# Optimization experiments

Measured on AMD Instinct MI355X. Metric: run time of the kernel, lower is better.

Reference implementation:

```python
import jax, jax.numpy as jnp
import numpy as np

N_STATE = 8
N_NEURONS = 64
EPS = 1e-4


def setup_inputs() -> dict:
    key = jax.random.key(0)
    ks = jax.random.split(key, 10)
    B = 524288
    return {
        "hidden_state": jax.random.normal(ks[0], (B, N_STATE), dtype=jnp.float32),
        "u": jax.random.normal(ks[1], (B, 6), dtype=jnp.float32),
        "X": jax.random.uniform(ks[2], (2 * N_STATE + N_NEURONS, 2 * N_STATE + N_NEURONS), dtype=jnp.float32),
        "calB_2": jax.random.uniform(ks[3], (N_STATE, 6), dtype=jnp.float32),
        "C_2": jax.random.uniform(ks[4], (5, N_STATE), dtype=jnp.float32),
        "calD_12": jax.random.uniform(ks[5], (N_NEURONS, 6), dtype=jnp.float32),
        "D_21": jax.random.uniform(ks[6], (5, N_NEURONS), dtype=jnp.float32),
        "D_22": jax.random.uniform(ks[7], (5, 6), dtype=jnp.float32),
        "Y_1": jax.random.uniform(ks[8], (N_STATE, N_STATE), dtype=jnp.float32),
        "biasvec": jax.random.uniform(ks[9], (N_STATE + N_NEURONS + 5,), dtype=jnp.float32),
    }


def _system_matrices(X, Y_1):
    s, n = N_STATE, N_NEURONS
    H = X.T @ X + EPS * jnp.eye(2 * s + n, dtype=X.dtype)
    F_ = H[s + n:, :s]
    B1 = H[s + n:, s:s + n]
    calP = H[s + n:, s + n:]
    C1 = -H[s:s + n, :s]
    H11 = H[:s, :s]
    E = 0.5 * (H11 + calP + Y_1)
    H22 = H[s:s + n, s:s + n]
    Lambda = 0.5 * jnp.diag(H22)
    D11 = -jnp.tril(H22, k=-1)
    return E, F_, B1, Lambda, C1, D11


def _calculate_w(x, u, C1, D11, calD_12, Lambda, bw):
    # Dtilde = diag(1/Lambda) @ D11 : strictly lower triangular -> forward substitution
    Dtilde = D11 / Lambda[:, None]
    rhs = x @ C1.T + u @ calD_12.T + bw  # (B, n)
    v0 = rhs / Lambda  # Linv @ rhs row-wise

    def step(v, args):
        i, dcol = args
        vi = jax.lax.dynamic_index_in_dim(v, i, axis=1, keepdims=False)  # (B,)
        return v + jnp.tanh(vi)[:, None] * dcol[None, :], None

    v, _ = jax.lax.scan(step, v0, (jnp.arange(N_NEURONS), Dtilde.T))
    return jnp.tanh(v)


def reference(hidden_state, u, X, calB_2, C_2, calD_12, D_21, D_22, Y_1, biasvec):
    s, n = N_STATE, N_NEURONS
    bx = biasvec[:s]
    bw = biasvec[s:s + n]
    by = biasvec[s + n:]
    E, F_, B1, Lambda, C1, D11 = _system_matrices(X, Y_1)
    Einv = jnp.linalg.inv(E)
    w = _calculate_w(hidden_state, u, C1, D11, calD_12, Lambda, bw)
    Ehidden = hidden_state @ F_.T + w @ B1.T + u @ calB_2.T + bx
    hidden = Ehidden @ Einv.T
    y = hidden_state @ C_2.T + w @ D_21.T + u @ D_22.T + by
    return hidden, y
```

## Files before the change

kernel.cpp:

```cpp
#include <hip/hip_runtime.h>
#include <hip/hip_fp16.h>
#include <math.h>


constexpr int NH = 80;

constexpr int WS_DTT2 = 0;
constexpr int WS_V0C  = 2048;
constexpr int WS_G2P  = 2560;
constexpr int WS_D21P = 2816;
constexpr int WS_BWF  = 2976;
constexpr int WS_G1   = 3040;
constexpr int WS_G3   = 3104;
constexpr int WS_G4   = 3152;
constexpr int WS_C2W  = 3160;
constexpr int WS_D22W = 3200;
constexpr int WS_BY   = 3232;
constexpr int WS_H    = 4096;
constexpr int WS_EINV = 10496;

__device__ __forceinline__ unsigned pack_rn(float a, float b) {
    unsigned lo = __half_as_ushort(__float2half(a));
    unsigned hi = __half_as_ushort(__float2half(b));
    return lo | (hi << 16);
}

typedef _Float16 h2 __attribute__((ext_vector_type(2)));

__device__ __forceinline__ float dot2(unsigned c, unsigned w, float acc) {
#if __has_builtin(__builtin_amdgcn_fdot2)
    return __builtin_amdgcn_fdot2(__builtin_bit_cast(h2, c),
                                  __builtin_bit_cast(h2, w), acc, false);
#else
    float out;
    asm("v_dot2_f32_f16 %0, %1, %2, %3" : "=v"(out) : "v"(c), "v"(w), "0"(acc));
    return out;
#endif
}
__device__ __forceinline__ float lo_f(unsigned u) { return (float)__builtin_bit_cast(h2, u).x; }
__device__ __forceinline__ float hi_f(unsigned u) { return (float)__builtin_bit_cast(h2, u).y; }

__global__ void k_gram(const float* __restrict__ X, float* __restrict__ ws) {
    int idx = blockIdx.x * blockDim.x + threadIdx.x;
    if (idx >= NH * NH) return;
    int a = idx / NH, b = idx % NH;
    float acc = (a == b) ? 1e-4f : 0.f;
    for (int k = 0; k < NH; k++) acc += X[k * NH + a] * X[k * NH + b];
    ws[WS_H + idx] = acc;
}

__global__ void k_solve(const float* __restrict__ Y1, float* __restrict__ ws) {
    __shared__ float sM[8][17];
    __shared__ int sPiv;
    int tid = threadIdx.x;
    const float* H = ws + WS_H;
    {
        int r = tid >> 4, c = tid & 15;
        sM[r][c] = (c < 8)
            ? 0.5f * (H[r * NH + c] + H[(72 + r) * NH + 72 + c] + Y1[r * 8 + c])
            : ((c - 8 == r) ? 1.f : 0.f);
    }
    __syncthreads();
    for (int p = 0; p < 8; p++) {
        if (tid == 0) {
            int pr = p; float best = fabsf(sM[p][p]);
            for (int r = p + 1; r < 8; r++) {
                float v = fabsf(sM[r][p]);
                if (v > best) { best = v; pr = r; }
            }
            sPiv = pr;
        }
        __syncthreads();
        int pr = sPiv;
        if (pr != p && tid < 16) { float tv = sM[p][tid]; sM[p][tid] = sM[pr][tid]; sM[pr][tid] = tv; }
        __syncthreads();
        if (tid < 16) {
            float inv = 1.f / sM[p][p];
            sM[p][tid] *= inv;
        }
        __syncthreads();
        int r = tid >> 4, c = tid & 15;
        float f = sM[r][p], pc = sM[p][c];
        __syncthreads();
        if (r != p) sM[r][c] -= f * pc;
        __syncthreads();
    }
    if (tid < 64) ws[WS_EINV + tid] = sM[tid >> 3][8 + (tid & 7)];
}

__global__ void k_finish(const float* __restrict__ calB2,
                         const float* __restrict__ calD12,
                         const float* __restrict__ C2,
                         const float* __restrict__ D21,
                         const float* __restrict__ D22,
                         const float* __restrict__ bias,
                         float* ws) {
    __shared__ float srL[64];
    __shared__ float sEinv[64];
    int tid = threadIdx.x;
    const float* H = ws + WS_H;
    unsigned* wsu = (unsigned*)ws;
    const float KAPPA = 2.8853900817779268f;

    if (tid < 64) srL[tid] = 2.0f / H[(8 + tid) * NH + 8 + tid];
    else if (tid < 128) sEinv[tid - 64] = ws[WS_EINV + tid - 64];
    __syncthreads();

    for (int idx = tid; idx < 2048; idx += 256) {
        int i = idx >> 5, p = idx & 31;
        int j0 = 2 * p, j1 = 2 * p + 1;
        float f0 = (j0 < i) ? -KAPPA * H[(8 + i) * NH + 8 + j0] * srL[i] : 0.f;
        float f1 = (j1 < i) ? -KAPPA * H[(8 + i) * NH + 8 + j1] * srL[i] : 0.f;
        wsu[WS_DTT2 + idx] = pack_rn(f0, f1);
    }
    for (int idx = tid; idx < 512; idx += 256) {
        int i = idx >> 3, c = idx & 7;
        float f0 = 0.f, f1 = 0.f;
        if (c < 4) {
            f0 = -KAPPA * H[(8 + i) * NH + 2 * c] * srL[i];
            f1 = -KAPPA * H[(8 + i) * NH + 2 * c + 1] * srL[i];
        } else if (c < 7) {
            int d = 2 * (c - 4);
            f0 = KAPPA * calD12[i * 6 + d] * srL[i];
            f1 = KAPPA * calD12[i * 6 + d + 1] * srL[i];
        }
        wsu[WS_V0C + idx] = pack_rn(f0, f1);
    }
    for (int idx = tid; idx < 256; idx += 256) {
        int a = idx >> 5, p = idx & 31;
        float g0 = 0.f, g1 = 0.f;
        for (int k = 0; k < 8; k++) {
            g0 += sEinv[a * 8 + k] * H[(72 + k) * NH + 8 + 2 * p];
            g1 += sEinv[a * 8 + k] * H[(72 + k) * NH + 8 + 2 * p + 1];
        }
        wsu[WS_G2P + idx] = pack_rn(g0, g1);
    }
    for (int idx = tid; idx < 160; idx += 256) {
        int q = idx / 32, p = idx % 32;
        wsu[WS_D21P + idx] = pack_rn(D21[q * 64 + 2 * p], D21[q * 64 + 2 * p + 1]);
    }
    if (tid < 64) ws[WS_BWF + tid] = KAPPA * bias[8 + tid] * srL[tid];
    if (tid < 64) {
        int a = tid >> 3, s = tid & 7; float acc = 0.f;
        for (int k = 0; k < 8; k++) acc += sEinv[a * 8 + k] * H[(72 + k) * NH + s];
        ws[WS_G1 + tid] = acc;
    }
    if (tid < 48) {
        int a = tid / 6, c = tid % 6; float acc = 0.f;
        for (int k = 0; k < 8; k++) acc += sEinv[a * 8 + k] * calB2[k * 6 + c];
        ws[WS_G3 + tid] = acc;
    }
    if (tid < 8) {
        float acc = 0.f;
        for (int k = 0; k < 8; k++) acc += sEinv[tid * 8 + k] * bias[k];
        ws[WS_G4 + tid] = acc;
    }
    if (tid < 40) ws[WS_C2W + tid] = C2[tid];
    if (tid < 30) ws[WS_D22W + tid] = D22[tid];
    if (tid < 5)  ws[WS_BY + tid]  = bias[72 + tid];
}

__device__ __forceinline__ float tanh_scaled(float q) {
    float e = __builtin_amdgcn_exp2f(q);
    return 1.f - 2.f * __builtin_amdgcn_rcpf(1.f + e);
}

__global__ __launch_bounds__(256) void k_main(
    const float* __restrict__ xg, const float* __restrict__ ug,
    const float* __restrict__ ws, float* __restrict__ out, int B)
{
    int t = blockIdx.x * blockDim.x + threadIdx.x;
    if (t >= B) return;

    const unsigned* wsu = (const unsigned*)ws;

    float xv[8], uv[6];
    {
        const float4* xp = reinterpret_cast<const float4*>(xg + (size_t)t * 8);
        float4 a0 = xp[0], a1 = xp[1];
        xv[0]=a0.x; xv[1]=a0.y; xv[2]=a0.z; xv[3]=a0.w;
        xv[4]=a1.x; xv[5]=a1.y; xv[6]=a1.z; xv[7]=a1.w;
        const float2* up = reinterpret_cast<const float2*>(ug + (size_t)t * 6);
        float2 c0 = up[0], c1 = up[1], c2 = up[2];
        uv[0]=c0.x; uv[1]=c0.y; uv[2]=c1.x; uv[3]=c1.y; uv[4]=c2.x; uv[5]=c2.y;
    }
    unsigned xh[4], uh[3];
    #pragma unroll
    for (int c = 0; c < 4; c++) xh[c] = pack_rn(xv[2 * c], xv[2 * c + 1]);
    #pragma unroll
    for (int c = 0; c < 3; c++) uh[c] = pack_rn(uv[2 * c], uv[2 * c + 1]);

    unsigned sv[32];
    #pragma unroll
    for (int k = 0; k < 32; k++) {
        float a0 = ws[WS_BWF + 2 * k];
        float a1 = ws[WS_BWF + 2 * k + 1];
        #pragma unroll
        for (int c = 0; c < 4; c++) {
            a0 = dot2(wsu[WS_V0C + (2 * k) * 8 + c],     xh[c], a0);
            a1 = dot2(wsu[WS_V0C + (2 * k + 1) * 8 + c], xh[c], a1);
        }
        #pragma unroll
        for (int c = 0; c < 3; c++) {
            a0 = dot2(wsu[WS_V0C + (2 * k) * 8 + 4 + c],     uh[c], a0);
            a1 = dot2(wsu[WS_V0C + (2 * k + 1) * 8 + 4 + c], uh[c], a1);
        }
        sv[k] = pack_rn(a0, a1);
    }

    float h[8];
    #pragma unroll
    for (int a = 0; a < 8; a++) {
        float acc = ws[WS_G4 + a];
        #pragma unroll
        for (int s = 0; s < 8; s++) acc += xv[s] * ws[WS_G1 + a * 8 + s];
        #pragma unroll
        for (int c = 0; c < 6; c++) acc += uv[c] * ws[WS_G3 + a * 6 + c];
        h[a] = acc;
    }
    float y[5];
    #pragma unroll
    for (int q = 0; q < 5; q++) {
        float acc = ws[WS_BY + q];
        #pragma unroll
        for (int s = 0; s < 8; s++) acc += xv[s] * ws[WS_C2W + q * 8 + s];
        #pragma unroll
        for (int c = 0; c < 6; c++) acc += uv[c] * ws[WS_D22W + q * 6 + c];
        y[q] = acc;
    }

    #pragma unroll
    for (int k = 0; k < 32; k++) {
        unsigned cur = sv[k];
        float acc = lo_f(cur);
        #pragma unroll
        for (int p = 0; p < k; p++) acc = dot2(wsu[WS_DTT2 + (2 * k) * 32 + p], sv[p], acc);
        float we = tanh_scaled(acc);

        float acc2 = hi_f(cur);
        #pragma unroll
        for (int p = 0; p < k; p++) acc2 = dot2(wsu[WS_DTT2 + (2 * k + 1) * 32 + p], sv[p], acc2);
        acc2 += lo_f(wsu[WS_DTT2 + (2 * k + 1) * 32 + k]) * we;
        float wo = tanh_scaled(acc2);

        sv[k] = pack_rn(we, wo);
    }

    #pragma unroll
    for (int a = 0; a < 8; a++) {
        float acc = h[a];
        #pragma unroll
        for (int p = 0; p < 32; p++) acc = dot2(wsu[WS_G2P + a * 32 + p], sv[p], acc);
        h[a] = acc;
    }
    float4* hp = reinterpret_cast<float4*>(out + (size_t)t * 8);
    hp[0] = make_float4(h[0], h[1], h[2], h[3]);
    hp[1] = make_float4(h[4], h[5], h[6], h[7]);

    float* yp = out + (size_t)B * 8 + (size_t)t * 5;
    #pragma unroll
    for (int q = 0; q < 5; q++) {
        float acc = y[q];
        #pragma unroll
        for (int p = 0; p < 32; p++) acc = dot2(wsu[WS_D21P + q * 32 + p], sv[p], acc);
        yp[q] = acc;
    }
}

extern "C" void kernel_launch(void* const* d_in, const int* in_sizes, int n_in,
                              void* d_out, int out_size, void* d_ws, size_t ws_size,
                              hipStream_t stream) {
    const float* x      = (const float*)d_in[0];
    const float* u      = (const float*)d_in[1];
    const float* X      = (const float*)d_in[2];
    const float* calB2  = (const float*)d_in[3];
    const float* C2     = (const float*)d_in[4];
    const float* calD12 = (const float*)d_in[5];
    const float* D21    = (const float*)d_in[6];
    const float* D22    = (const float*)d_in[7];
    const float* Y1     = (const float*)d_in[8];
    const float* bias   = (const float*)d_in[9];
    float* ws  = (float*)d_ws;
    float* out = (float*)d_out;
    int B = in_sizes[0] / 8;

    k_gram  <<<(NH * NH + 255) / 256, 256, 0, stream>>>(X, ws);
    k_solve <<<1, 128, 0, stream>>>(Y1, ws);
    k_finish<<<1, 256, 0, stream>>>(calB2, calD12, C2, D21, D22, bias, ws);
    k_main  <<<(B + 255) / 256, 256, 0, stream>>>(x, u, ws, out, B);
}
```

Measured before the change: 77.86 us.

## Merge solve and finish kernels, pack h/y weights to fp16 dot2, split accumulators

Fuses the single-block inverse solve and the weight-preparation kernel into one launch, which removes one kernel launch and a workspace round trip for Einv. The x/u contributions to h and y are now computed with packed fp16 dot2 instructions instead of fp32 FMAs, which cuts ALU work and register use but lowers precision on those terms. The triangular recurrence also splits each dot chain into even and odd accumulators to shorten the dependency chains.

```diff
diff --git a/kernel.cpp b/kernel.cpp
--- a/kernel.cpp
+++ b/kernel.cpp
@@ -9,15 +9,14 @@
 constexpr int WS_V0C  = 2048;
 constexpr int WS_G2P  = 2560;
 constexpr int WS_D21P = 2816;
-constexpr int WS_BWF  = 2976;
-constexpr int WS_G1   = 3040;
-constexpr int WS_G3   = 3104;
-constexpr int WS_G4   = 3152;
-constexpr int WS_C2W  = 3160;
-constexpr int WS_D22W = 3200;
-constexpr int WS_BY   = 3232;
+constexpr int WS_G1P  = 2976;
+constexpr int WS_G3P  = 3008;
+constexpr int WS_C2P  = 3032;
+constexpr int WS_D22P = 3052;
+constexpr int WS_BWF  = 3072;
+constexpr int WS_G4   = 3136;
+constexpr int WS_BY   = 3144;
 constexpr int WS_H    = 4096;
-constexpr int WS_EINV = 10496;
 
 __device__ __forceinline__ unsigned pack_rn(float a, float b) {
     unsigned lo = __half_as_ushort(__float2half(a));
@@ -49,18 +48,32 @@
     ws[WS_H + idx] = acc;
 }
 
-__global__ void k_solve(const float* __restrict__ Y1, float* __restrict__ ws) {
+__global__ void k_prep(const float* __restrict__ calB2,
+                       const float* __restrict__ calD12,
+                       const float* __restrict__ C2,
+                       const float* __restrict__ D21,
+                       const float* __restrict__ D22,
+                       const float* __restrict__ Y1,
+                       const float* __restrict__ bias,
+                       float* ws) {
     __shared__ float sM[8][17];
     __shared__ int sPiv;
+    __shared__ float srL[64];
+    __shared__ float sEinv[64];
     int tid = threadIdx.x;
     const float* H = ws + WS_H;
-    {
+    unsigned* wsu = (unsigned*)ws;
+    const float KAPPA = 2.8853900817779268f;
+
+    if (tid < 128) {
         int r = tid >> 4, c = tid & 15;
         sM[r][c] = (c < 8)
             ? 0.5f * (H[r * NH + c] + H[(72 + r) * NH + 72 + c] + Y1[r * 8 + c])
             : ((c - 8 == r) ? 1.f : 0.f);
     }
+    if (tid >= 128 && tid < 192) srL[tid - 128] = 2.0f / H[(8 + tid - 128) * NH + 8 + tid - 128];
     __syncthreads();
+
     for (int p = 0; p < 8; p++) {
         if (tid == 0) {
             int pr = p; float best = fabsf(sM[p][p]);
@@ -79,31 +92,13 @@
             sM[p][tid] *= inv;
         }
         __syncthreads();
-        int r = tid >> 4, c = tid & 15;
-        float f = sM[r][p], pc = sM[p][c];
-        __syncthreads();
-        if (r != p) sM[r][c] -= f * pc;
-        __syncthreads();
-    }
-    if (tid < 64) ws[WS_EINV + tid] = sM[tid >> 3][8 + (tid & 7)];
-}
-
-__global__ void k_finish(const float* __restrict__ calB2,
-                         const float* __restrict__ calD12,
-                         const float* __restrict__ C2,
-                         const float* __restrict__ D21,
-                         const float* __restrict__ D22,
-                         const float* __restrict__ bias,
-                         float* ws) {
-    __shared__ float srL[64];
-    __shared__ float sEinv[64];
-    int tid = threadIdx.x;
-    const float* H = ws + WS_H;
-    unsigned* wsu = (unsigned*)ws;
-    const float KAPPA = 2.8853900817779268f;
-
-    if (tid < 64) srL[tid] = 2.0f / H[(8 + tid) * NH + 8 + tid];
-    else if (tid < 128) sEinv[tid - 64] = ws[WS_EINV + tid - 64];
+        float f = 0.f, pc = 0.f;
+        if (tid < 128) { int r = tid >> 4, c = tid & 15; f = sM[r][p]; pc = sM[p][c]; }
+        __syncthreads();
+        if (tid < 128) { int r = tid >> 4, c = tid & 15; if (r != p) sM[r][c] -= f * pc; }
+        __syncthreads();
+    }
+    if (tid < 64) sEinv[tid] = sM[tid >> 3][8 + (tid & 7)];
     __syncthreads();
 
     for (int idx = tid; idx < 2048; idx += 256) {
@@ -126,38 +121,52 @@
         }
         wsu[WS_V0C + idx] = pack_rn(f0, f1);
     }
-    for (int idx = tid; idx < 256; idx += 256) {
-        int a = idx >> 5, p = idx & 31;
+    if (tid < 256) {
+        int a = tid >> 5, p = tid & 31;
         float g0 = 0.f, g1 = 0.f;
         for (int k = 0; k < 8; k++) {
             g0 += sEinv[a * 8 + k] * H[(72 + k) * NH + 8 + 2 * p];
             g1 += sEinv[a * 8 + k] * H[(72 + k) * NH + 8 + 2 * p + 1];
         }
-        wsu[WS_G2P + idx] = pack_rn(g0, g1);
-    }
-    for (int idx = tid; idx < 160; idx += 256) {
-        int q = idx / 32, p = idx % 32;
-        wsu[WS_D21P + idx] = pack_rn(D21[q * 64 + 2 * p], D21[q * 64 + 2 * p + 1]);
+        wsu[WS_G2P + tid] = pack_rn(g0, g1);
+    }
+    if (tid < 160) {
+        int q = tid / 32, p = tid % 32;
+        wsu[WS_D21P + tid] = pack_rn(D21[q * 64 + 2 * p], D21[q * 64 + 2 * p + 1]);
+    }
+    if (tid < 32) {
+        int a = tid >> 2, c = tid & 3;
+        float g0 = 0.f, g1 = 0.f;
+        for (int k = 0; k < 8; k++) {
+            g0 += sEinv[a * 8 + k] * H[(72 + k) * NH + 2 * c];
+            g1 += sEinv[a * 8 + k] * H[(72 + k) * NH + 2 * c + 1];
+        }
+        wsu[WS_G1P + tid] = pack_rn(g0, g1);
+    }
+    if (tid < 24) {
+        int a = tid / 3, c = tid % 3;
+        float g0 = 0.f, g1 = 0.f;
+        for (int k = 0; k < 8; k++) {
+            g0 += sEinv[a * 8 + k] * calB2[k * 6 + 2 * c];
+            g1 += sEinv[a * 8 + k] * calB2[k * 6 + 2 * c + 1];
+        }
+        wsu[WS_G3P + tid] = pack_rn(g0, g1);
+    }
+    if (tid < 20) {
+        int q = tid >> 2, c = tid & 3;
+        wsu[WS_C2P + tid] = pack_rn(C2[q * 8 + 2 * c], C2[q * 8 + 2 * c + 1]);
+    }
+    if (tid < 15) {
+        int q = tid / 3, c = tid % 3;
+        wsu[WS_D22P + tid] = pack_rn(D22[q * 6 + 2 * c], D22[q * 6 + 2 * c + 1]);
     }
     if (tid < 64) ws[WS_BWF + tid] = KAPPA * bias[8 + tid] * srL[tid];
-    if (tid < 64) {
-        int a = tid >> 3, s = tid & 7; float acc = 0.f;
-        for (int k = 0; k < 8; k++) acc += sEinv[a * 8 + k] * H[(72 + k) * NH + s];
-        ws[WS_G1 + tid] = acc;
-    }
-    if (tid < 48) {
-        int a = tid / 6, c = tid % 6; float acc = 0.f;
-        for (int k = 0; k < 8; k++) acc += sEinv[a * 8 + k] * calB2[k * 6 + c];
-        ws[WS_G3 + tid] = acc;
-    }
     if (tid < 8) {
         float acc = 0.f;
         for (int k = 0; k < 8; k++) acc += sEinv[tid * 8 + k] * bias[k];
         ws[WS_G4 + tid] = acc;
     }
-    if (tid < 40) ws[WS_C2W + tid] = C2[tid];
-    if (tid < 30) ws[WS_D22W + tid] = D22[tid];
-    if (tid < 5)  ws[WS_BY + tid]  = bias[72 + tid];
+    if (tid < 5) ws[WS_BY + tid] = bias[72 + tid];
 }
 
 __device__ __forceinline__ float tanh_scaled(float q) {
@@ -174,21 +183,16 @@
 
     const unsigned* wsu = (const unsigned*)ws;
 
-    float xv[8], uv[6];
+    unsigned xh[4], uh[3];
     {
         const float4* xp = reinterpret_cast<const float4*>(xg + (size_t)t * 8);
         float4 a0 = xp[0], a1 = xp[1];
-        xv[0]=a0.x; xv[1]=a0.y; xv[2]=a0.z; xv[3]=a0.w;
-        xv[4]=a1.x; xv[5]=a1.y; xv[6]=a1.z; xv[7]=a1.w;
+        xh[0] = pack_rn(a0.x, a0.y); xh[1] = pack_rn(a0.z, a0.w);
+        xh[2] = pack_rn(a1.x, a1.y); xh[3] = pack_rn(a1.z, a1.w);
         const float2* up = reinterpret_cast<const float2*>(ug + (size_t)t * 6);
         float2 c0 = up[0], c1 = up[1], c2 = up[2];
-        uv[0]=c0.x; uv[1]=c0.y; uv[2]=c1.x; uv[3]=c1.y; uv[4]=c2.x; uv[5]=c2.y;
-    }
-    unsigned xh[4], uh[3];
-    #pragma unroll
-    for (int c = 0; c < 4; c++) xh[c] = pack_rn(xv[2 * c], xv[2 * c + 1]);
-    #pragma unroll
-    for (int c = 0; c < 3; c++) uh[c] = pack_rn(uv[2 * c], uv[2 * c + 1]);
+        uh[0] = pack_rn(c0.x, c0.y); uh[1] = pack_rn(c1.x, c1.y); uh[2] = pack_rn(c2.x, c2.y);
+    }
 
     unsigned sv[32];
     #pragma unroll
@@ -213,9 +217,9 @@
     for (int a = 0; a < 8; a++) {
         float acc = ws[WS_G4 + a];
         #pragma unroll
-        for (int s = 0; s < 8; s++) acc += xv[s] * ws[WS_G1 + a * 8 + s];
-        #pragma unroll
-        for (int c = 0; c < 6; c++) acc += uv[c] * ws[WS_G3 + a * 6 + c];
+        for (int c = 0; c < 4; c++) acc = dot2(wsu[WS_G1P + a * 4 + c], xh[c], acc);
+        #pragma unroll
+        for (int c = 0; c < 3; c++) acc = dot2(wsu[WS_G3P + a * 3 + c], uh[c], acc);
         h[a] = acc;
     }
     float y[5];
@@ -223,25 +227,29 @@
     for (int q = 0; q < 5; q++) {
         float acc = ws[WS_BY + q];
         #pragma unroll
-        for (int s = 0; s < 8; s++) acc += xv[s] * ws[WS_C2W + q * 8 + s];
-        #pragma unroll
-        for (int c = 0; c < 6; c++) acc += uv[c] * ws[WS_D22W + q * 6 + c];
+        for (int c = 0; c < 4; c++) acc = dot2(wsu[WS_C2P + q * 4 + c], xh[c], acc);
+        #pragma unroll
+        for (int c = 0; c < 3; c++) acc = dot2(wsu[WS_D22P + q * 3 + c], uh[c], acc);
         y[q] = acc;
     }
 
     #pragma unroll
     for (int k = 0; k < 32; k++) {
         unsigned cur = sv[k];
-        float acc = lo_f(cur);
-        #pragma unroll
-        for (int p = 0; p < k; p++) acc = dot2(wsu[WS_DTT2 + (2 * k) * 32 + p], sv[p], acc);
-        float we = tanh_scaled(acc);
-
-        float acc2 = hi_f(cur);
-        #pragma unroll
-        for (int p = 0; p < k; p++) acc2 = dot2(wsu[WS_DTT2 + (2 * k + 1) * 32 + p], sv[p], acc2);
-        acc2 += lo_f(wsu[WS_DTT2 + (2 * k + 1) * 32 + k]) * we;
-        float wo = tanh_scaled(acc2);
+
+        float aE = lo_f(cur), aO = 0.f;
+        #pragma unroll
+        for (int p = 0; p < k; p += 2) aE = dot2(wsu[WS_DTT2 + (2 * k) * 32 + p], sv[p], aE);
+        #pragma unroll
+        for (int p = 1; p < k; p += 2) aO = dot2(wsu[WS_DTT2 + (2 * k) * 32 + p], sv[p], aO);
+        float we = tanh_scaled(aE + aO);
+
+        float bE = hi_f(cur), bO = 0.f;
+        #pragma unroll
+        for (int p = 0; p < k; p += 2) bE = dot2(wsu[WS_DTT2 + (2 * k + 1) * 32 + p], sv[p], bE);
+        #pragma unroll
+        for (int p = 1; p < k; p += 2) bO = dot2(wsu[WS_DTT2 + (2 * k + 1) * 32 + p], sv[p], bO);
+        float wo = tanh_scaled(bE + bO + lo_f(wsu[WS_DTT2 + (2 * k + 1) * 32 + k]) * we);
 
         sv[k] = pack_rn(we, wo);
     }
@@ -284,8 +292,7 @@
     float* out = (float*)d_out;
     int B = in_sizes[0] / 8;
 
-    k_gram  <<<(NH * NH + 255) / 256, 256, 0, stream>>>(X, ws);
-    k_solve <<<1, 128, 0, stream>>>(Y1, ws);
-    k_finish<<<1, 256, 0, stream>>>(calB2, calD12, C2, D21, D22, bias, ws);
-    k_main  <<<(B + 255) / 256, 256, 0, stream>>>(x, u, ws, out, B);
-}
+    k_gram<<<(NH * NH + 255) / 256, 256, 0, stream>>>(X, ws);
+    k_prep<<<1, 256, 0, stream>>>(calB2, calD12, C2, D21, D22, Y1, bias, ws);
+    k_main<<<(B + 255) / 256, 256, 0, stream>>>(x, u, ws, out, B);
+}
```

Result: faster. 71.56 us (-8.1%).
